# Optimization experiments

Hardware: AMD Instinct MI355X
Metric: run time of the kernel (lower is better)

Reference implementation:

```python
import jax, jax.numpy as jnp
import numpy as np

N_EMBD = 1024
N_HEAD = 16

def setup_inputs() -> dict:
    key = jax.random.key(0)
    ks = jax.random.split(key, 5)
    B, T, C = 4, 2048, N_EMBD
    scale = 1.0 / np.sqrt(C)
    return {
        "x": jax.random.normal(ks[0], (B, T, C), dtype=jnp.float32),
        "w_qkv": jax.random.normal(ks[1], (C, 3 * C), dtype=jnp.float32) * scale,
        "b_qkv": jax.random.normal(ks[2], (3 * C,), dtype=jnp.float32) * 0.02,
        "w_proj": jax.random.normal(ks[3], (C, C), dtype=jnp.float32) * scale,
        "b_proj": jax.random.normal(ks[4], (C,), dtype=jnp.float32) * 0.02,
    }

def reference(x, w_qkv, b_qkv, w_proj, b_proj):
    B, T, C = x.shape
    H = N_HEAD
    D = C // H  # head dim
    qkv = x @ w_qkv + b_qkv  # [B,T,3C]
    q, k, v = jnp.split(qkv, 3, axis=-1)
    # [B,T,C] -> [B,H,T,D]
    q = q.reshape(B, T, H, D).transpose(0, 2, 1, 3)
    k = k.reshape(B, T, H, D).transpose(0, 2, 1, 3)
    v = v.reshape(B, T, H, D).transpose(0, 2, 1, 3)
    att = jnp.einsum("bhqd,bhkd->bhqk", q, k) / jnp.sqrt(jnp.asarray(D, x.dtype))
    causal = jnp.tril(jnp.ones((T, T), dtype=bool))  # [T,T]
    att = jnp.where(causal[None, None, :, :], att, -jnp.inf)
    att = jax.nn.softmax(att, axis=-1)
    y = jnp.einsum("bhqk,bhkd->bhqd", att, v)  # [B,H,T,D]
    y = y.transpose(0, 2, 1, 3).reshape(B, T, C)
    return y @ w_proj + b_proj
```

## Files before the change

kernel.cpp:

```cpp
#include <hip/hip_runtime.h>
#include <hip/hip_bf16.h>
#include <stdint.h>

typedef __bf16 bf16_8 __attribute__((ext_vector_type(8)));
typedef float f32_4 __attribute__((ext_vector_type(4)));
typedef short short4v __attribute__((ext_vector_type(4)));

static __device__ __forceinline__ unsigned short f2bf(float f) {
    union { float f; unsigned int u; } v; v.f = f;
    unsigned int u = v.u;
    unsigned int r = (u + 0x7fffu + ((u >> 16) & 1u)) >> 16;
    return (unsigned short)r;
}

static __device__ __forceinline__ unsigned int pack_bf16x2(float a, float b) {
    union { float f; unsigned int u; } ua, ub;
    ua.f = a; ub.f = b;
    return __builtin_amdgcn_perm(ub.u + 0x8000u, ua.u + 0x8000u, 0x07060302u);
}

static __device__ __forceinline__ f32_4 mfma_16x16x16_bf16(short4v a, short4v b, f32_4 c) {
#if __has_builtin(__builtin_amdgcn_mfma_f32_16x16x16bf16_1k)
    return __builtin_amdgcn_mfma_f32_16x16x16bf16_1k(a, b, c, 0, 0, 0);
#else
    asm volatile("v_mfma_f32_16x16x16_bf16 %0, %1, %2, %0"
                 : "+v"(c) : "v"(a), "v"(b));
    return c;
#endif
}

static __device__ __forceinline__ void gll16(const unsigned short* g, unsigned short* l) {
    __builtin_amdgcn_global_load_lds(
        (const __attribute__((address_space(1))) unsigned int*)g,
        (__attribute__((address_space(3))) unsigned int*)l, 16, 0, 0);
}

__global__ void cvt_bf16_kernel(const float* __restrict__ in,
                                unsigned int* __restrict__ out, int n4) {
    int i = blockIdx.x * blockDim.x + threadIdx.x;
    if (i < n4) {
        float4 f = ((const float4*)in)[i];
        uint2 o;
        o.x = pack_bf16x2(f.x, f.y);
        o.y = pack_bf16x2(f.z, f.w);
        ((uint2*)out)[i] = o;
    }
}

__global__ void transpose_cvt_kernel(const float* __restrict__ in,
                                     unsigned short* __restrict__ out,
                                     int K, int N) {
    __shared__ unsigned short tile[64][65];
    int k0 = blockIdx.y * 64, n0 = blockIdx.x * 64;
    int tc = threadIdx.x & 63, tr = threadIdx.x >> 6;
    for (int p = 0; p < 16; ++p) {
        int k = p * 4 + tr;
        tile[k][tc] = f2bf(in[(size_t)(k0 + k) * N + n0 + tc]);
    }
    __syncthreads();
    for (int p = 0; p < 16; ++p) {
        int n = p * 4 + tr;
        out[(size_t)(n0 + n) * K + k0 + tc] = tile[tc][n];
    }
}

#define BK 32
#define QSCALE 0.1803368801111204f

__global__ __launch_bounds__(256) void gemm_qkv(
    const unsigned short* __restrict__ A,
    const unsigned short* __restrict__ Bt,
    const float* __restrict__ bias,
    int M, int N, int K,
    unsigned short* __restrict__ q_out, unsigned short* __restrict__ k_out,
    unsigned short* __restrict__ v_out) {
    __shared__ __align__(16) unsigned short As[128 * BK];
    __shared__ __align__(16) unsigned short Bs[128 * BK];
    int tid = threadIdx.x;
    int wave = tid >> 6, lane = tid & 63;
    int wm = wave & 1, wn = wave >> 1;
    int quad = lane >> 4, l16 = lane & 15;
    int m0 = blockIdx.y * 128, n0 = blockIdx.x * 128;
    int which = n0 >> 10;

    f32_4 acc[4][4] = {};

    int lrow = lane >> 2;
    int lcol = (lane & 3) * 8;
    const unsigned short* Ag = A + (size_t)(m0 + wave * 32 + lrow) * K + lcol;
    const unsigned short* Bg = Bt + (size_t)(n0 + wave * 32 + lrow) * K + lcol;
    unsigned short* Asl = As + wave * 32 * BK;
    unsigned short* Bsl = Bs + wave * 32 * BK;

    if (which < 2) {
        for (int kt = 0; kt < K; kt += BK) {
            gll16(Ag + kt, Asl);
            gll16(Ag + kt + (size_t)16 * K, Asl + 16 * BK);
            gll16(Bg + kt, Bsl);
            gll16(Bg + kt + (size_t)16 * K, Bsl + 16 * BK);
            __syncthreads();
            bf16_8 af[4], bfr[4];
            for (int i = 0; i < 4; ++i)
                af[i] = *(const bf16_8*)(As + (wm * 64 + i * 16 + l16) * BK + quad * 8);
            for (int j = 0; j < 4; ++j)
                bfr[j] = *(const bf16_8*)(Bs + (wn * 64 + j * 16 + l16) * BK + quad * 8);
            for (int i = 0; i < 4; ++i)
                for (int j = 0; j < 4; ++j)
                    acc[i][j] = __builtin_amdgcn_mfma_f32_16x16x32_bf16(
                        bfr[j], af[i], acc[i][j], 0, 0, 0);
            __syncthreads();
        }
    } else {
        for (int kt = 0; kt < K; kt += BK) {
            gll16(Ag + kt, Asl);
            gll16(Ag + kt + (size_t)16 * K, Asl + 16 * BK);
            gll16(Bg + kt, Bsl);
            gll16(Bg + kt + (size_t)16 * K, Bsl + 16 * BK);
            __syncthreads();
            bf16_8 af[4], bfr[4];
            for (int i = 0; i < 4; ++i)
                af[i] = *(const bf16_8*)(As + (wm * 64 + i * 16 + l16) * BK + quad * 8);
            for (int j = 0; j < 4; ++j)
                bfr[j] = *(const bf16_8*)(Bs + (wn * 64 + j * 16 + l16) * BK + quad * 8);
            for (int i = 0; i < 4; ++i)
                for (int j = 0; j < 4; ++j)
                    acc[i][j] = __builtin_amdgcn_mfma_f32_16x16x32_bf16(
                        af[i], bfr[j], acc[i][j], 0, 0, 0);
            __syncthreads();
        }
    }

    int b = m0 >> 11;
    int tbase = (m0 & 2047) + wm * 64;
    int nw0 = n0 + wn * 64;
    if (which < 2) {
        unsigned short* dst = which == 0 ? q_out : k_out;
        float scale = which == 0 ? QSCALE : 1.0f;
        int h0 = ((n0 & 1023) >> 6) + wn;
        size_t base = ((size_t)((b << 4) + h0) * 2048) * 64;
        for (int j = 0; j < 4; ++j) {
            float4 b4 = *(const float4*)(bias + nw0 + j * 16 + quad * 4);
            int d0 = j * 16 + quad * 4;
            for (int i = 0; i < 4; ++i) {
                int t = tbase + i * 16 + l16;
                uint2 pk;
                pk.x = pack_bf16x2((acc[i][j][0] + b4.x) * scale,
                                   (acc[i][j][1] + b4.y) * scale);
                pk.y = pack_bf16x2((acc[i][j][2] + b4.z) * scale,
                                   (acc[i][j][3] + b4.w) * scale);
                *(uint2*)(dst + base + (size_t)t * 64 + d0) = pk;
            }
        }
    } else {
        for (int j = 0; j < 4; ++j) {
            int n = nw0 + j * 16 + l16;
            int c = n & 1023, h = c >> 6, d = c & 63;
            float bs = bias[n];
            size_t base = ((size_t)((b << 4) + h) * 64 + d) * 2048;
            for (int i = 0; i < 4; ++i) {
                int t0 = tbase + i * 16 + quad * 4;
                uint2 pk;
                pk.x = pack_bf16x2(acc[i][j][0] + bs, acc[i][j][1] + bs);
                pk.y = pack_bf16x2(acc[i][j][2] + bs, acc[i][j][3] + bs);
                *(uint2*)(v_out + base + t0) = pk;
            }
        }
    }
}

__global__ __launch_bounds__(256) void gemm_proj(
    const unsigned short* __restrict__ A,
    const unsigned short* __restrict__ Bt,
    const float* __restrict__ bias,
    int M, int N, int K, float* __restrict__ outf) {
    __shared__ __align__(16) unsigned short As[128 * BK];
    __shared__ __align__(16) unsigned short Bs[64 * BK];
    int tid = threadIdx.x;
    int wave = tid >> 6, lane = tid & 63;
    int wm = wave & 1, wn = wave >> 1;
    int quad = lane >> 4, l16 = lane & 15;
    int m0 = blockIdx.y * 128, n0 = blockIdx.x * 64;

    f32_4 acc[4][2] = {};

    int lrow = lane >> 2;
    int lcol = (lane & 3) * 8;
    const unsigned short* Ag = A + (size_t)(m0 + wave * 32 + lrow) * K + lcol;
    const unsigned short* Bg = Bt + (size_t)(n0 + wave * 16 + lrow) * K + lcol;
    unsigned short* Asl = As + wave * 32 * BK;
    unsigned short* Bsl = Bs + wave * 16 * BK;

    for (int kt = 0; kt < K; kt += BK) {
        gll16(Ag + kt, Asl);
        gll16(Ag + kt + (size_t)16 * K, Asl + 16 * BK);
        gll16(Bg + kt, Bsl);
        __syncthreads();
        bf16_8 af[4], bfr[2];
        for (int i = 0; i < 4; ++i)
            af[i] = *(const bf16_8*)(As + (wm * 64 + i * 16 + l16) * BK + quad * 8);
        for (int j = 0; j < 2; ++j)
            bfr[j] = *(const bf16_8*)(Bs + (wn * 32 + j * 16 + l16) * BK + quad * 8);
        for (int i = 0; i < 4; ++i)
            for (int j = 0; j < 2; ++j)
                acc[i][j] = __builtin_amdgcn_mfma_f32_16x16x32_bf16(
                    af[i], bfr[j], acc[i][j], 0, 0, 0);
        __syncthreads();
    }

    for (int j = 0; j < 2; ++j) {
        int n = n0 + wn * 32 + j * 16 + l16;
        float bs = bias[n];
        for (int i = 0; i < 4; ++i) {
            int m = m0 + wm * 64 + i * 16 + quad * 4;
            for (int r = 0; r < 4; ++r)
                outf[(size_t)(m + r) * N + n] = acc[i][j][r] + bs;
        }
    }
}

#define KSTR 72

__global__ __launch_bounds__(256, 4) void attn_kernel(
    const unsigned short* __restrict__ Q, const unsigned short* __restrict__ Kb,
    const unsigned short* __restrict__ Vt, unsigned short* __restrict__ Y,
    int T) {
    __shared__ __align__(16) unsigned short KsB[2][64 * KSTR];
    __shared__ __align__(16) unsigned short VtsB[2][64 * KSTR];

    int tid = threadIdx.x;
    int wave = tid >> 6, lane = tid & 63;
    int quad = lane >> 4, l16 = lane & 15;
    int bh = blockIdx.x;
    int b = bh >> 4, h = bh & 15;

    int srow = tid >> 2;
    int schunk = (tid & 3) * 16;
    const unsigned short* Kg = Kb + ((size_t)bh * T + srow) * 64 + schunk;
    const unsigned short* Vg = Vt + ((size_t)bh * 64 + srow) * (size_t)T + schunk;

    for (int phase = 0; phase < 2; ++phase) {
        int qt = phase == 0 ? (16 + blockIdx.y) : (15 - blockIdx.y);
        int qw = qt * 64 + wave * 16;
        int nkt = qt + 1;

        bf16_8 qa[2];
        for (int ks = 0; ks < 2; ++ks)
            qa[ks] = *(const bf16_8*)(Q + ((size_t)bh * T + qw + l16) * 64 +
                                      ks * 32 + quad * 8);

        f32_4 o[4] = {};
        float lsum = 0.0f;

        {
            uint4 k0 = *(const uint4*)(Kg);
            uint4 k1 = *(const uint4*)(Kg + 8);
            uint4 v0 = *(const uint4*)(Vg);
            uint4 v1 = *(const uint4*)(Vg + 8);
            *(uint4*)(&KsB[0][srow * KSTR + schunk]) = k0;
            *(uint4*)(&KsB[0][srow * KSTR + schunk + 8]) = k1;
            *(uint4*)(&VtsB[0][srow * KSTR + schunk]) = v0;
            *(uint4*)(&VtsB[0][srow * KSTR + schunk + 8]) = v1;
        }
        __syncthreads();

        for (int kt = 0; kt < nkt; ++kt) {
            int cur = kt & 1;
            int kb = kt * 64;
            bool more = (kt + 1) < nkt;

            uint4 nk0, nk1, nv0, nv1;
            if (more) {
                const unsigned short* kp = Kg + (size_t)(kt + 1) * 4096;
                nk0 = *(const uint4*)kp;
                nk1 = *(const uint4*)(kp + 8);
                const unsigned short* vp = Vg + (kt + 1) * 64;
                nv0 = *(const uint4*)vp;
                nv1 = *(const uint4*)(vp + 8);
            }

            const unsigned short* KsC = KsB[cur];
            const unsigned short* VtsC = VtsB[cur];

            bf16_8 ka[4][2];
            for (int kf = 0; kf < 4; ++kf)
                for (int ks = 0; ks < 2; ++ks)
                    ka[kf][ks] = *(const bf16_8*)(KsC + (kf * 16 + l16) * KSTR + ks * 32 + quad * 8);

            f32_4 s[4] = {};
            for (int kf = 0; kf < 4; ++kf) {
                s[kf] = __builtin_amdgcn_mfma_f32_16x16x32_bf16(ka[kf][0], qa[0], s[kf], 0, 0, 0);
                s[kf] = __builtin_amdgcn_mfma_f32_16x16x32_bf16(ka[kf][1], qa[1], s[kf], 0, 0, 0);
            }

            if (kt == qt) {
                int q = qw + l16;
                for (int kf = 0; kf < 4; ++kf) {
                    int kk = kb + kf * 16 + quad * 4;
                    for (int r = 0; r < 4; ++r)
                        if (kk + r > q) s[kf][r] = -1e30f;
                }
            }

            float rsum = 0.0f;
            for (int kf = 0; kf < 4; ++kf)
                for (int r = 0; r < 4; ++r) {
                    float p = __builtin_amdgcn_exp2f(s[kf][r]);
                    s[kf][r] = p;
                    rsum += p;
                }
            rsum += __shfl_xor(rsum, 16);
            rsum += __shfl_xor(rsum, 32);
            lsum += rsum;

            short4v pb[4];
            for (int kf = 0; kf < 4; ++kf) {
                union { unsigned int u[2]; short4v s4; } pu;
                pu.u[0] = pack_bf16x2(s[kf][0], s[kf][1]);
                pu.u[1] = pack_bf16x2(s[kf][2], s[kf][3]);
                pb[kf] = pu.s4;
            }
            for (int kf = 0; kf < 4; ++kf)
                for (int df = 0; df < 4; ++df) {
                    short4v va = *(const short4v*)(VtsC + (df * 16 + l16) * KSTR + kf * 16 + quad * 4);
                    o[df] = mfma_16x16x16_bf16(va, pb[kf], o[df]);
                }

            if (more) {
                int nxt = cur ^ 1;
                *(uint4*)(&KsB[nxt][srow * KSTR + schunk]) = nk0;
                *(uint4*)(&KsB[nxt][srow * KSTR + schunk + 8]) = nk1;
                *(uint4*)(&VtsB[nxt][srow * KSTR + schunk]) = nv0;
                *(uint4*)(&VtsB[nxt][srow * KSTR + schunk + 8]) = nv1;
            }
            __syncthreads();
        }

        float inv = 1.0f / lsum;
        unsigned short* yp = Y + ((size_t)b * T + qw + l16) * 1024 + h * 64 + quad * 4;
        for (int df = 0; df < 4; ++df) {
            uint2 pk;
            pk.x = pack_bf16x2(o[df][0] * inv, o[df][1] * inv);
            pk.y = pack_bf16x2(o[df][2] * inv, o[df][3] * inv);
            *(uint2*)(yp + df * 16) = pk;
        }
    }
}

extern "C" void kernel_launch(void* const* d_in, const int* in_sizes, int n_in,
                              void* d_out, int out_size, void* d_ws, size_t ws_size,
                              hipStream_t stream) {
    const float* x = (const float*)d_in[0];
    const float* w_qkv = (const float*)d_in[1];
    const float* b_qkv = (const float*)d_in[2];
    const float* w_proj = (const float*)d_in[3];
    const float* b_proj = (const float*)d_in[4];
    float* out = (float*)d_out;

    unsigned short* xbf = (unsigned short*)d_ws;
    unsigned short* wqkvt = xbf + 8388608;
    unsigned short* wprojt = wqkvt + 3145728;
    unsigned short* Qb = wprojt + 1048576;
    unsigned short* Kb = Qb + 8388608;
    unsigned short* Vtb = Kb + 8388608;
    unsigned short* Yb = Vtb + 8388608;

    hipLaunchKernelGGL(cvt_bf16_kernel, dim3(8192), dim3(256), 0, stream,
                       x, (unsigned int*)xbf, 2097152);
    hipLaunchKernelGGL(transpose_cvt_kernel, dim3(48, 16), dim3(256), 0, stream,
                       w_qkv, wqkvt, 1024, 3072);
    hipLaunchKernelGGL(transpose_cvt_kernel, dim3(16, 16), dim3(256), 0, stream,
                       w_proj, wprojt, 1024, 1024);
    hipLaunchKernelGGL(gemm_qkv, dim3(24, 64), dim3(256), 0, stream,
                       xbf, wqkvt, b_qkv, 8192, 3072, 1024,
                       Qb, Kb, Vtb);
    hipLaunchKernelGGL(attn_kernel, dim3(64, 16), dim3(256), 0, stream,
                       Qb, Kb, Vtb, Yb, 2048);
    hipLaunchKernelGGL(gemm_proj, dim3(16, 64), dim3(256), 0, stream,
                       Yb, wprojt, b_proj, 8192, 1024, 1024, out);
}
```

Before: 279.0 us.

## Fuse prep kernels, widen GEMM K-tile with swizzled LDS, restructure attention to share K/V

```diff
diff --git a/kernel.cpp b/kernel.cpp
--- a/kernel.cpp
+++ b/kernel.cpp
@@ -35,23 +35,31 @@
         (__attribute__((address_space(3))) unsigned int*)l, 16, 0, 0);
 }
 
-__global__ void cvt_bf16_kernel(const float* __restrict__ in,
-                                unsigned int* __restrict__ out, int n4) {
-    int i = blockIdx.x * blockDim.x + threadIdx.x;
-    if (i < n4) {
-        float4 f = ((const float4*)in)[i];
+__global__ __launch_bounds__(256) void prep_kernel(
+    const float* __restrict__ x, unsigned int* __restrict__ xbf,
+    const float* __restrict__ w_qkv, unsigned short* __restrict__ wqkvt,
+    const float* __restrict__ w_proj, unsigned short* __restrict__ wprojt) {
+    __shared__ unsigned short tile[64][65];
+    int bid = blockIdx.x;
+    if (bid < 8192) {
+        int i = bid * 256 + threadIdx.x;
+        float4 f = ((const float4*)x)[i];
         uint2 o;
         o.x = pack_bf16x2(f.x, f.y);
         o.y = pack_bf16x2(f.z, f.w);
-        ((uint2*)out)[i] = o;
-    }
-}
-
-__global__ void transpose_cvt_kernel(const float* __restrict__ in,
-                                     unsigned short* __restrict__ out,
-                                     int K, int N) {
-    __shared__ unsigned short tile[64][65];
-    int k0 = blockIdx.y * 64, n0 = blockIdx.x * 64;
+        ((uint2*)xbf)[i] = o;
+        return;
+    }
+    const float* in; unsigned short* out; int N, bx, by;
+    if (bid < 8960) {
+        in = w_qkv; out = wqkvt; N = 3072;
+        int t = bid - 8192; bx = t % 48; by = t / 48;
+    } else {
+        in = w_proj; out = wprojt; N = 1024;
+        int t = bid - 8960; bx = t & 15; by = t >> 4;
+    }
+    const int K = 1024;
+    int k0 = by * 64, n0 = bx * 64;
     int tc = threadIdx.x & 63, tr = threadIdx.x >> 6;
     for (int p = 0; p < 16; ++p) {
         int k = p * 4 + tr;
@@ -64,7 +72,7 @@
     }
 }
 
-#define BK 32
+#define BK 64
 #define QSCALE 0.1803368801111204f
 
 __global__ __launch_bounds__(256) void gemm_qkv(
@@ -85,49 +93,43 @@
 
     f32_4 acc[4][4] = {};
 
-    int lrow = lane >> 2;
-    int lcol = (lane & 3) * 8;
-    const unsigned short* Ag = A + (size_t)(m0 + wave * 32 + lrow) * K + lcol;
-    const unsigned short* Bg = Bt + (size_t)(n0 + wave * 32 + lrow) * K + lcol;
+    int srow = lane >> 3;
+    int scs = ((lane & 7) ^ srow) * 8;
+    const unsigned short* Ag = A + (size_t)(m0 + wave * 32 + srow) * K + scs;
+    const unsigned short* Bg = Bt + (size_t)(n0 + wave * 32 + srow) * K + scs;
     unsigned short* Asl = As + wave * 32 * BK;
     unsigned short* Bsl = Bs + wave * 32 * BK;
-
-    if (which < 2) {
-        for (int kt = 0; kt < K; kt += BK) {
-            gll16(Ag + kt, Asl);
-            gll16(Ag + kt + (size_t)16 * K, Asl + 16 * BK);
-            gll16(Bg + kt, Bsl);
-            gll16(Bg + kt + (size_t)16 * K, Bsl + 16 * BK);
-            __syncthreads();
-            bf16_8 af[4], bfr[4];
+    int sx = l16 & 7;
+
+    for (int kt = 0; kt < K; kt += BK) {
+        for (int p = 0; p < 4; ++p) {
+            gll16(Ag + kt + (size_t)(8 * p) * K, Asl + p * 8 * BK);
+            gll16(Bg + kt + (size_t)(8 * p) * K, Bsl + p * 8 * BK);
+        }
+        __syncthreads();
+        bf16_8 af[4][2], bfr[4][2];
+        for (int i = 0; i < 4; ++i)
+            for (int ks = 0; ks < 2; ++ks)
+                af[i][ks] = *(const bf16_8*)(As + (wm * 64 + i * 16 + l16) * BK +
+                                             ((unsigned)((ks * 4 + quad) ^ sx)) * 8);
+        for (int j = 0; j < 4; ++j)
+            for (int ks = 0; ks < 2; ++ks)
+                bfr[j][ks] = *(const bf16_8*)(Bs + (wn * 64 + j * 16 + l16) * BK +
+                                              ((unsigned)((ks * 4 + quad) ^ sx)) * 8);
+        if (which < 2) {
             for (int i = 0; i < 4; ++i)
-                af[i] = *(const bf16_8*)(As + (wm * 64 + i * 16 + l16) * BK + quad * 8);
-            for (int j = 0; j < 4; ++j)
-                bfr[j] = *(const bf16_8*)(Bs + (wn * 64 + j * 16 + l16) * BK + quad * 8);
+                for (int j = 0; j < 4; ++j) {
+                    acc[i][j] = __builtin_amdgcn_mfma_f32_16x16x32_bf16(bfr[j][0], af[i][0], acc[i][j], 0, 0, 0);
+                    acc[i][j] = __builtin_amdgcn_mfma_f32_16x16x32_bf16(bfr[j][1], af[i][1], acc[i][j], 0, 0, 0);
+                }
+        } else {
             for (int i = 0; i < 4; ++i)
-                for (int j = 0; j < 4; ++j)
-                    acc[i][j] = __builtin_amdgcn_mfma_f32_16x16x32_bf16(
-                        bfr[j], af[i], acc[i][j], 0, 0, 0);
-            __syncthreads();
-        }
-    } else {
-        for (int kt = 0; kt < K; kt += BK) {
-            gll16(Ag + kt, Asl);
-            gll16(Ag + kt + (size_t)16 * K, Asl + 16 * BK);
-            gll16(Bg + kt, Bsl);
-            gll16(Bg + kt + (size_t)16 * K, Bsl + 16 * BK);
-            __syncthreads();
-            bf16_8 af[4], bfr[4];
-            for (int i = 0; i < 4; ++i)
-                af[i] = *(const bf16_8*)(As + (wm * 64 + i * 16 + l16) * BK + quad * 8);
-            for (int j = 0; j < 4; ++j)
-                bfr[j] = *(const bf16_8*)(Bs + (wn * 64 + j * 16 + l16) * BK + quad * 8);
-            for (int i = 0; i < 4; ++i)
-                for (int j = 0; j < 4; ++j)
-                    acc[i][j] = __builtin_amdgcn_mfma_f32_16x16x32_bf16(
-                        af[i], bfr[j], acc[i][j], 0, 0, 0);
-            __syncthreads();
-        }
+                for (int j = 0; j < 4; ++j) {
+                    acc[i][j] = __builtin_amdgcn_mfma_f32_16x16x32_bf16(af[i][0], bfr[j][0], acc[i][j], 0, 0, 0);
+                    acc[i][j] = __builtin_amdgcn_mfma_f32_16x16x32_bf16(af[i][1], bfr[j][1], acc[i][j], 0, 0, 0);
+                }
+        }
+        __syncthreads();
     }
 
     int b = m0 >> 11;
@@ -183,27 +185,34 @@
 
     f32_4 acc[4][2] = {};
 
-    int lrow = lane >> 2;
-    int lcol = (lane & 3) * 8;
-    const unsigned short* Ag = A + (size_t)(m0 + wave * 32 + lrow) * K + lcol;
-    const unsigned short* Bg = Bt + (size_t)(n0 + wave * 16 + lrow) * K + lcol;
+    int srow = lane >> 3;
+    int scs = ((lane & 7) ^ srow) * 8;
+    const unsigned short* Ag = A + (size_t)(m0 + wave * 32 + srow) * K + scs;
+    const unsigned short* Bg = Bt + (size_t)(n0 + wave * 16 + srow) * K + scs;
     unsigned short* Asl = As + wave * 32 * BK;
     unsigned short* Bsl = Bs + wave * 16 * BK;
+    int sx = l16 & 7;
 
     for (int kt = 0; kt < K; kt += BK) {
-        gll16(Ag + kt, Asl);
-        gll16(Ag + kt + (size_t)16 * K, Asl + 16 * BK);
-        gll16(Bg + kt, Bsl);
+        for (int p = 0; p < 4; ++p)
+            gll16(Ag + kt + (size_t)(8 * p) * K, Asl + p * 8 * BK);
+        for (int p = 0; p < 2; ++p)
+            gll16(Bg + kt + (size_t)(8 * p) * K, Bsl + p * 8 * BK);
         __syncthreads();
-        bf16_8 af[4], bfr[2];
+        bf16_8 af[4][2], bfr[2][2];
         for (int i = 0; i < 4; ++i)
-            af[i] = *(const bf16_8*)(As + (wm * 64 + i * 16 + l16) * BK + quad * 8);
+            for (int ks = 0; ks < 2; ++ks)
+                af[i][ks] = *(const bf16_8*)(As + (wm * 64 + i * 16 + l16) * BK +
+                                             ((unsigned)((ks * 4 + quad) ^ sx)) * 8);
         for (int j = 0; j < 2; ++j)
-            bfr[j] = *(const bf16_8*)(Bs + (wn * 32 + j * 16 + l16) * BK + quad * 8);
+            for (int ks = 0; ks < 2; ++ks)
+                bfr[j][ks] = *(const bf16_8*)(Bs + (wn * 32 + j * 16 + l16) * BK +
+                                              ((unsigned)((ks * 4 + quad) ^ sx)) * 8);
         for (int i = 0; i < 4; ++i)
-            for (int j = 0; j < 2; ++j)
-                acc[i][j] = __builtin_amdgcn_mfma_f32_16x16x32_bf16(
-                    af[i], bfr[j], acc[i][j], 0, 0, 0);
+            for (int j = 0; j < 2; ++j) {
+                acc[i][j] = __builtin_amdgcn_mfma_f32_16x16x32_bf16(af[i][0], bfr[j][0], acc[i][j], 0, 0, 0);
+                acc[i][j] = __builtin_amdgcn_mfma_f32_16x16x32_bf16(af[i][1], bfr[j][1], acc[i][j], 0, 0, 0);
+            }
         __syncthreads();
     }
 
@@ -218,129 +227,147 @@
     }
 }
 
-#define KSTR 72
-
 __global__ __launch_bounds__(256, 4) void attn_kernel(
     const unsigned short* __restrict__ Q, const unsigned short* __restrict__ Kb,
     const unsigned short* __restrict__ Vt, unsigned short* __restrict__ Y,
     int T) {
-    __shared__ __align__(16) unsigned short KsB[2][64 * KSTR];
-    __shared__ __align__(16) unsigned short VtsB[2][64 * KSTR];
+    __shared__ __align__(16) unsigned short KsB[2][64 * 64];
+    __shared__ __align__(16) unsigned short VtsB[2][64 * 64];
 
     int tid = threadIdx.x;
     int wave = tid >> 6, lane = tid & 63;
     int quad = lane >> 4, l16 = lane & 15;
     int bh = blockIdx.x;
     int b = bh >> 4, h = bh & 15;
-
-    int srow = tid >> 2;
-    int schunk = (tid & 3) * 16;
-    const unsigned short* Kg = Kb + ((size_t)bh * T + srow) * 64 + schunk;
-    const unsigned short* Vg = Vt + ((size_t)bh * 64 + srow) * (size_t)T + schunk;
-
-    for (int phase = 0; phase < 2; ++phase) {
-        int qt = phase == 0 ? (16 + blockIdx.y) : (15 - blockIdx.y);
-        int qw = qt * 64 + wave * 16;
-        int nkt = qt + 1;
-
-        bf16_8 qa[2];
-        for (int ks = 0; ks < 2; ++ks)
-            qa[ks] = *(const bf16_8*)(Q + ((size_t)bh * T + qw + l16) * 64 +
-                                      ks * 32 + quad * 8);
-
-        f32_4 o[4] = {};
-        float lsum = 0.0f;
-
+    int y = blockIdx.y;
+    int qtA = 31 - y, qtB = y;
+    int qwA = qtA * 64 + wave * 16;
+    int qwB = qtB * 64 + wave * 16;
+
+    int srow = lane >> 3;
+    int scs = ((lane & 7) ^ srow) * 8;
+    int sx = l16 & 7;
+
+    bf16_8 qaA[2], qaB[2];
+    for (int ks = 0; ks < 2; ++ks) {
+        qaA[ks] = *(const bf16_8*)(Q + ((size_t)bh * T + qwA + l16) * 64 + ks * 32 + quad * 8);
+        qaB[ks] = *(const bf16_8*)(Q + ((size_t)bh * T + qwB + l16) * 64 + ks * 32 + quad * 8);
+    }
+
+    f32_4 oA[4] = {}, oB[4] = {};
+    float lsA = 0.0f, lsB = 0.0f;
+
+    int nkt = qtA + 1;
+
+    for (int p = 0; p < 2; ++p) {
+        int row = wave * 16 + p * 8;
+        gll16(Kb + ((size_t)bh * T + row + srow) * 64 + scs, &KsB[0][row * 64]);
+        gll16(Vt + ((size_t)bh * 64 + row + srow) * (size_t)T + scs, &VtsB[0][row * 64]);
+    }
+    __syncthreads();
+
+    for (int kt = 0; kt < nkt; ++kt) {
+        int cur = kt & 1;
+        int kb = kt * 64;
+        if (kt + 1 < nkt) {
+            int kb2 = kb + 64, nxt = cur ^ 1;
+            for (int p = 0; p < 2; ++p) {
+                int row = wave * 16 + p * 8;
+                gll16(Kb + ((size_t)bh * T + kb2 + row + srow) * 64 + scs, &KsB[nxt][row * 64]);
+                gll16(Vt + ((size_t)bh * 64 + row + srow) * (size_t)T + kb2 + scs, &VtsB[nxt][row * 64]);
+            }
+        }
+        const unsigned short* KsC = KsB[cur];
+        const unsigned short* VtsC = VtsB[cur];
+        bool doB = (kt <= qtB);
+
+        f32_4 sA[4] = {}, sB[4] = {};
+        for (int kf = 0; kf < 4; ++kf) {
+            bf16_8 k0 = *(const bf16_8*)(KsC + (kf * 16 + l16) * 64 + ((unsigned)(quad ^ sx)) * 8);
+            bf16_8 k1 = *(const bf16_8*)(KsC + (kf * 16 + l16) * 64 + ((unsigned)((4 + quad) ^ sx)) * 8);
+            sA[kf] = __builtin_amdgcn_mfma_f32_16x16x32_bf16(k0, qaA[0], sA[kf], 0, 0, 0);
+            sA[kf] = __builtin_amdgcn_mfma_f32_16x16x32_bf16(k1, qaA[1], sA[kf], 0, 0, 0);
+            if (doB) {
+                sB[kf] = __builtin_amdgcn_mfma_f32_16x16x32_bf16(k0, qaB[0], sB[kf], 0, 0, 0);
+                sB[kf] = __builtin_amdgcn_mfma_f32_16x16x32_bf16(k1, qaB[1], sB[kf], 0, 0, 0);
+            }
+        }
+
+        if (kt == qtA) {
+            int q = qwA + l16;
+            for (int kf = 0; kf < 4; ++kf) {
+                int kk = kb + kf * 16 + quad * 4;
+                for (int r = 0; r < 4; ++r)
+                    if (kk + r > q) sA[kf][r] = -1e30f;
+            }
+        }
+        if (kt == qtB) {
+            int q = qwB + l16;
+            for (int kf = 0; kf < 4; ++kf) {
+                int kk = kb + kf * 16 + quad * 4;
+                for (int r = 0; r < 4; ++r)
+                    if (kk + r > q) sB[kf][r] = -1e30f;
+            }
+        }
+
+        short4v pbA[4], pbB[4];
         {
-            uint4 k0 = *(const uint4*)(Kg);
-            uint4 k1 = *(const uint4*)(Kg + 8);
-            uint4 v0 = *(const uint4*)(Vg);
-            uint4 v1 = *(const uint4*)(Vg + 8);
-            *(uint4*)(&KsB[0][srow * KSTR + schunk]) = k0;
-            *(uint4*)(&KsB[0][srow * KSTR + schunk + 8]) = k1;
-            *(uint4*)(&VtsB[0][srow * KSTR + schunk]) = v0;
-            *(uint4*)(&VtsB[0][srow * KSTR + schunk + 8]) = v1;
+            float rs = 0.0f;
+            for (int kf = 0; kf < 4; ++kf) {
+                f32_4 p;
+                for (int r = 0; r < 4; ++r) { p[r] = __builtin_amdgcn_exp2f(sA[kf][r]); rs += p[r]; }
+                union { unsigned int u[2]; short4v s4; } pu;
+                pu.u[0] = pack_bf16x2(p[0], p[1]);
+                pu.u[1] = pack_bf16x2(p[2], p[3]);
+                pbA[kf] = pu.s4;
+            }
+            rs += __shfl_xor(rs, 16);
+            rs += __shfl_xor(rs, 32);
+            lsA += rs;
+        }
+        if (doB) {
+            float rs = 0.0f;
+            for (int kf = 0; kf < 4; ++kf) {
+                f32_4 p;
+                for (int r = 0; r < 4; ++r) { p[r] = __builtin_amdgcn_exp2f(sB[kf][r]); rs += p[r]; }
+                union { unsigned int u[2]; short4v s4; } pu;
+                pu.u[0] = pack_bf16x2(p[0], p[1]);
+                pu.u[1] = pack_bf16x2(p[2], p[3]);
+                pbB[kf] = pu.s4;
+            }
+            rs += __shfl_xor(rs, 16);
+            rs += __shfl_xor(rs, 32);
+            lsB += rs;
+        }
+
+        for (int kf = 0; kf < 4; ++kf) {
+            unsigned voff = ((unsigned)((2 * kf + (quad >> 1)) ^ sx)) * 8 + (quad & 1) * 4;
+            for (int df = 0; df < 4; ++df) {
+                short4v va = *(const short4v*)(VtsC + (df * 16 + l16) * 64 + voff);
+                oA[df] = mfma_16x16x16_bf16(va, pbA[kf], oA[df]);
+                if (doB) oB[df] = mfma_16x16x16_bf16(va, pbB[kf], oB[df]);
+            }
         }
         __syncthreads();
-
-        for (int kt = 0; kt < nkt; ++kt) {
-            int cur = kt & 1;
-            int kb = kt * 64;
-            bool more = (kt + 1) < nkt;
-
-            uint4 nk0, nk1, nv0, nv1;
-            if (more) {
-                const unsigned short* kp = Kg + (size_t)(kt + 1) * 4096;
-                nk0 = *(const uint4*)kp;
-                nk1 = *(const uint4*)(kp + 8);
-                const unsigned short* vp = Vg + (kt + 1) * 64;
-                nv0 = *(const uint4*)vp;
-                nv1 = *(const uint4*)(vp + 8);
-            }
-
-            const unsigned short* KsC = KsB[cur];
-            const unsigned short* VtsC = VtsB[cur];
-
-            bf16_8 ka[4][2];
-            for (int kf = 0; kf < 4; ++kf)
-                for (int ks = 0; ks < 2; ++ks)
-                    ka[kf][ks] = *(const bf16_8*)(KsC + (kf * 16 + l16) * KSTR + ks * 32 + quad * 8);
-
-            f32_4 s[4] = {};
-            for (int kf = 0; kf < 4; ++kf) {
-                s[kf] = __builtin_amdgcn_mfma_f32_16x16x32_bf16(ka[kf][0], qa[0], s[kf], 0, 0, 0);
-                s[kf] = __builtin_amdgcn_mfma_f32_16x16x32_bf16(ka[kf][1], qa[1], s[kf], 0, 0, 0);
-            }
-
-            if (kt == qt) {
-                int q = qw + l16;
-                for (int kf = 0; kf < 4; ++kf) {
-                    int kk = kb + kf * 16 + quad * 4;
-                    for (int r = 0; r < 4; ++r)
-                        if (kk + r > q) s[kf][r] = -1e30f;
-                }
-            }
-
-            float rsum = 0.0f;
-            for (int kf = 0; kf < 4; ++kf)
-                for (int r = 0; r < 4; ++r) {
-                    float p = __builtin_amdgcn_exp2f(s[kf][r]);
-                    s[kf][r] = p;
-                    rsum += p;
-                }
-            rsum += __shfl_xor(rsum, 16);
-            rsum += __shfl_xor(rsum, 32);
-            lsum += rsum;
-
-            short4v pb[4];
-            for (int kf = 0; kf < 4; ++kf) {
-                union { unsigned int u[2]; short4v s4; } pu;
-                pu.u[0] = pack_bf16x2(s[kf][0], s[kf][1]);
-                pu.u[1] = pack_bf16x2(s[kf][2], s[kf][3]);
-                pb[kf] = pu.s4;
-            }
-            for (int kf = 0; kf < 4; ++kf)
-                for (int df = 0; df < 4; ++df) {
-                    short4v va = *(const short4v*)(VtsC + (df * 16 + l16) * KSTR + kf * 16 + quad * 4);
-                    o[df] = mfma_16x16x16_bf16(va, pb[kf], o[df]);
-                }
-
-            if (more) {
-                int nxt = cur ^ 1;
-                *(uint4*)(&KsB[nxt][srow * KSTR + schunk]) = nk0;
-                *(uint4*)(&KsB[nxt][srow * KSTR + schunk + 8]) = nk1;
-                *(uint4*)(&VtsB[nxt][srow * KSTR + schunk]) = nv0;
-                *(uint4*)(&VtsB[nxt][srow * KSTR + schunk + 8]) = nv1;
-            }
-            __syncthreads();
-        }
-
-        float inv = 1.0f / lsum;
-        unsigned short* yp = Y + ((size_t)b * T + qw + l16) * 1024 + h * 64 + quad * 4;
+    }
+
+    {
+        float inv = 1.0f / lsA;
+        unsigned short* yp = Y + ((size_t)b * T + qwA + l16) * 1024 + h * 64 + quad * 4;
         for (int df = 0; df < 4; ++df) {
             uint2 pk;
-            pk.x = pack_bf16x2(o[df][0] * inv, o[df][1] * inv);
-            pk.y = pack_bf16x2(o[df][2] * inv, o[df][3] * inv);
+            pk.x = pack_bf16x2(oA[df][0] * inv, oA[df][1] * inv);
+            pk.y = pack_bf16x2(oA[df][2] * inv, oA[df][3] * inv);
+            *(uint2*)(yp + df * 16) = pk;
+        }
+    }
+    {
+        float inv = 1.0f / lsB;
+        unsigned short* yp = Y + ((size_t)b * T + qwB + l16) * 1024 + h * 64 + quad * 4;
+        for (int df = 0; df < 4; ++df) {
+            uint2 pk;
+            pk.x = pack_bf16x2(oB[df][0] * inv, oB[df][1] * inv);
+            pk.y = pack_bf16x2(oB[df][2] * inv, oB[df][3] * inv);
             *(uint2*)(yp + df * 16) = pk;
         }
     }
@@ -364,12 +391,8 @@
     unsigned short* Vtb = Kb + 8388608;
     unsigned short* Yb = Vtb + 8388608;
 
-    hipLaunchKernelGGL(cvt_bf16_kernel, dim3(8192), dim3(256), 0, stream,
-                       x, (unsigned int*)xbf, 2097152);
-    hipLaunchKernelGGL(transpose_cvt_kernel, dim3(48, 16), dim3(256), 0, stream,
-                       w_qkv, wqkvt, 1024, 3072);
-    hipLaunchKernelGGL(transpose_cvt_kernel, dim3(16, 16), dim3(256), 0, stream,
-                       w_proj, wprojt, 1024, 1024);
+    hipLaunchKernelGGL(prep_kernel, dim3(9216), dim3(256), 0, stream,
+                       x, (unsigned int*)xbf, w_qkv, wqkvt, w_proj, wprojt);
     hipLaunchKernelGGL(gemm_qkv, dim3(24, 64), dim3(256), 0, stream,
                        xbf, wqkvt, b_qkv, 8192, 3072, 1024,
                        Qb, Kb, Vtb);
```

Measured after the change: 289.1 us. +3.6%, slower.
